# Kernel optimization log

Measured on AMD Instinct MI355X. Metric: run time of the kernel, lower is better.

Reference implementation:

```python
import jax, jax.numpy as jnp
import numpy as np

E4M3_MAX = 448.0
IGNORE = -1000.0
ROTARY_BASE = 10000.0


def quant_dequant_e4m3(w):
    """Emulate per-tensor FP8 E4M3 quantize->dequantize (3 mantissa bits, max 448)."""
    amax = jnp.max(jnp.abs(w))
    scale = E4M3_MAX / jnp.maximum(amax, 1e-12)
    v = w * scale
    a = jnp.abs(v)
    # exponent clipped to E4M3 range (min normal exp -6, max 8)
    e = jnp.clip(jnp.floor(jnp.log2(jnp.maximum(a, 1e-30))), -6.0, 8.0)
    step = jnp.exp2(e - 3.0)  # 3 mantissa bits
    q = jnp.clip(jnp.round(v / step) * step, -E4M3_MAX, E4M3_MAX)
    return (q / scale).astype(w.dtype)


def rotary_sin_cos(rotary_dim, n_ctx):
    pos = jnp.arange(n_ctx, dtype=jnp.float32)
    dim = jnp.arange(rotary_dim // 2, dtype=jnp.float32)
    inv_freq = ROTARY_BASE ** (-dim / (rotary_dim / 2))
    ang = pos[:, None] * inv_freq[None, :]            # [n_ctx, rotary_dim//2]
    ang = jnp.concatenate([ang, ang], axis=-1)        # [n_ctx, rotary_dim]
    return jnp.sin(ang), jnp.cos(ang)


def apply_rotary(x, sin, cos, rotary_dim):
    # x: [B, S, H, Dh]; rotate first rotary_dim dims with rotate-half convention
    S = x.shape[1]
    x_rot, x_pass = x[..., :rotary_dim], x[..., rotary_dim:]
    half = rotary_dim // 2
    x_flip = jnp.concatenate([-x_rot[..., half:], x_rot[..., :half]], axis=-1)
    c = cos[:S][None, :, None, :]
    s = sin[:S][None, :, None, :]
    out = x_rot * c + x_flip * s
    return jnp.concatenate([out, x_pass], axis=-1) if rotary_dim < x.shape[-1] else out


def setup_inputs() -> dict:
    key = jax.random.key(0)
    ks = jax.random.split(key, 8)
    B, S, D, H, Dh = 2, 2048, 1024, 16, 64
    return {
        "query_input": jax.random.normal(ks[0], (B, S, D), jnp.float32),
        "key_input": jax.random.normal(ks[1], (B, S, D), jnp.float32),
        "value_input": jax.random.normal(ks[2], (B, S, D), jnp.float32),
        "W_Q": jax.random.normal(ks[3], (H, D, Dh), jnp.float32) * 0.02,
        "W_K": jax.random.normal(ks[4], (H, D, Dh), jnp.float32) * 0.02,
        "W_V": jax.random.normal(ks[5], (H, D, Dh), jnp.float32) * 0.02,
        "W_O": jax.random.normal(ks[6], (H, Dh, D), jnp.float32) * 0.02,
        "b_Q": jnp.zeros((H, Dh), jnp.float32),
        "b_K": jnp.zeros((H, Dh), jnp.float32),
        "b_V": jnp.zeros((H, Dh), jnp.float32),
        "b_O": jnp.zeros((D,), jnp.float32),
    }


def reference(query_input, key_input, value_input, W_Q, W_K, W_V, W_O, b_Q, b_K, b_V, b_O):
    B, S, D = query_input.shape
    H, _, Dh = W_Q.shape
    rotary_dim = Dh
    attn_scale = jnp.sqrt(jnp.asarray(Dh, jnp.float32))

    # FP8-quantized QKV weights/biases (E4M3 quant-dequant emulation)
    Wq = quant_dequant_e4m3(W_Q)
    Wk = quant_dequant_e4m3(W_K)
    Wv = quant_dequant_e4m3(W_V)
    bq = quant_dequant_e4m3(b_Q)
    bk = quant_dequant_e4m3(b_K)
    bv = quant_dequant_e4m3(b_V)

    q = jnp.einsum("bsd,hde->bshe", query_input, Wq) + bq  # [B,S,H,Dh]
    k = jnp.einsum("bsd,hde->bshe", key_input, Wk) + bk
    v = jnp.einsum("bsd,hde->bshe", value_input, Wv) + bv

    sin, cos = rotary_sin_cos(rotary_dim, S)
    q = apply_rotary(q, sin, cos, rotary_dim)
    k = apply_rotary(k, sin, cos, rotary_dim)

    scores = jnp.einsum("bqhe,bkhe->bhqk", q, k) / attn_scale  # [B,H,S,S]
    causal = jnp.tril(jnp.ones((S, S), bool))
    scores = jnp.where(causal[None, None], scores, IGNORE)
    pattern = jax.nn.softmax(scores, axis=-1)

    z = jnp.einsum("bhqk,bkhe->bqhe", pattern, v)             # [B,S,H,Dh]
    out = jnp.einsum("bqhe,hed->bqd", z, W_O) + b_O           # [B,S,D]
    return out
```

## Files before the change

### kernel.cpp

```cpp
#include <hip/hip_runtime.h>
#include <math.h>


typedef __attribute__((ext_vector_type(8))) short bf16x8;
typedef __attribute__((ext_vector_type(16))) float f32x16;
typedef __attribute__((ext_vector_type(4))) float f32x4;
typedef __attribute__((ext_vector_type(4))) float f4;

#define E4M3_MAX 448.0f

__device__ inline float bf2f(ushort u) { return __uint_as_float(((unsigned)u) << 16); }
__device__ inline ushort f2bf(float f) {
  unsigned u = __float_as_uint(f);
  return (ushort)((u + 0x7FFF + ((u >> 16) & 1)) >> 16);
}
__device__ inline unsigned pack2bf(float a, float b) {
  unsigned ua = __float_as_uint(a), ub = __float_as_uint(b);
  return ((ua + 0x8000u) >> 16) | ((ub + 0x8000u) & 0xFFFF0000u);
}

__device__ __forceinline__ void gll16(const ushort* g, ushort* l) {
  __builtin_amdgcn_global_load_lds(
      (const __attribute__((address_space(1))) unsigned int*)g,
      (__attribute__((address_space(3))) unsigned int*)l, 16, 0, 0);
}

__device__ inline float qdq_qval(float w, float amax) {
  float scale = E4M3_MAX / fmaxf(amax, 1e-12f);
  float v = w * scale;
  float a = fmaxf(fabsf(v), 1e-30f);
  int ex;
  (void)frexpf(a, &ex);
  float e = fminf(fmaxf((float)(ex - 1), -6.0f), 8.0f);
  float step = exp2f(e - 3.0f);
  float q = rintf(v / step) * step;
  return fminf(fmaxf(q, -E4M3_MAX), E4M3_MAX);
}

__device__ __forceinline__ float redpart64(const float* __restrict__ p, int tid) {
  float v = p[tid & 63];
  #pragma unroll
  for (int o = 32; o > 0; o >>= 1) v = fmaxf(v, __shfl_xor(v, o));
  return v;
}

__global__ __launch_bounds__(256) void prep1(const float* __restrict__ W0,
                                             const float* __restrict__ W1,
                                             const float* __restrict__ W2,
                                             const float* __restrict__ b0,
                                             const float* __restrict__ b1,
                                             const float* __restrict__ b2,
                                             const float* __restrict__ Xq,
                                             const float* __restrict__ Xk,
                                             const float* __restrict__ Xv,
                                             float* __restrict__ amaxpart,
                                             ushort* __restrict__ xq,
                                             ushort* __restrict__ xk,
                                             ushort* __restrict__ xv) {
  __shared__ float wred[4];
  int bid = blockIdx.x, tid = threadIdx.x;
  if (bid < 384) {
    int y = bid >> 6, xb = bid & 63;
    const float* src = (y == 0) ? W0 : (y == 1) ? W1 : (y == 2) ? W2
                     : (y == 3) ? b0 : (y == 4) ? b1 : b2;
    int n = (y < 3) ? 1048576 : 1024;
    float m = 0.0f;
    for (int i = xb * 256 + tid; i < n; i += 64 * 256)
      m = fmaxf(m, fabsf(src[i]));
    #pragma unroll
    for (int off = 32; off > 0; off >>= 1)
      m = fmaxf(m, __shfl_xor(m, off));
    if ((tid & 63) == 0) wred[tid >> 6] = m;
    __syncthreads();
    if (tid == 0)
      amaxpart[y * 64 + xb] = fmaxf(fmaxf(wred[0], wred[1]), fmaxf(wred[2], wred[3]));
  } else {
    int t = bid - 384;
    int y = t >> 12, xb = t & 4095;
    const float* in = (y == 0) ? Xq : (y == 1) ? Xk : Xv;
    ushort* out = (y == 0) ? xq : (y == 1) ? xk : xv;
    int i = xb * 256 + tid;
    f4 v = *(const f4*)(in + (size_t)i * 4);
    uint2 o;
    o.x = (unsigned)f2bf(v[0]) | ((unsigned)f2bf(v[1]) << 16);
    o.y = (unsigned)f2bf(v[2]) | ((unsigned)f2bf(v[3]) << 16);
    *(uint2*)(out + (size_t)i * 4) = o;
  }
}

__global__ __launch_bounds__(256) void prep2(const float* __restrict__ W0,
                                             const float* __restrict__ W1,
                                             const float* __restrict__ W2,
                                             const float* __restrict__ WO,
                                             const float* __restrict__ b0,
                                             const float* __restrict__ b1,
                                             const float* __restrict__ b2,
                                             const float* __restrict__ amaxpart,
                                             float* __restrict__ amax,
                                             ushort* __restrict__ o0,
                                             ushort* __restrict__ o1,
                                             ushort* __restrict__ o2,
                                             ushort* __restrict__ woT,
                                             float* __restrict__ bq,
                                             float* __restrict__ bk,
                                             float* __restrict__ bv) {
  __shared__ float tile[64][65];
  int bid = blockIdx.x, tid = threadIdx.x;
  if (bid < 768) {
    int z = bid >> 8, r = bid & 255, hh = r >> 4, xb = r & 15;
    const float* W = (z == 0) ? W0 : (z == 1) ? W1 : W2;
    ushort* Bt = (z == 0) ? o0 : (z == 1) ? o1 : o2;
    float am = redpart64(amaxpart + z * 64, tid);
    if (r == 0 && tid == 0) amax[z] = am;
    int d0 = xb * 64;
    int e = tid & 63, dd = tid >> 6;
    #pragma unroll
    for (int p = 0; p < 16; p++)
      tile[dd + p * 4][e] = W[(size_t)hh * 65536 + (size_t)(d0 + dd + p * 4) * 64 + e];
    __syncthreads();
    int d = tid & 63, ee = tid >> 6;
    #pragma unroll
    for (int p = 0; p < 16; p++) {
      int e2 = ee + p * 4;
      Bt[(size_t)(hh * 64 + e2) * 1024 + d0 + d] = f2bf(qdq_qval(tile[d][e2], am));
    }
  } else if (bid < 780) {
    int q = bid - 768, y = q >> 2, xb = q & 3;
    const float* b = (y == 0) ? b0 : (y == 1) ? b1 : b2;
    float* o = (y == 0) ? bq : (y == 1) ? bk : bv;
    float am = redpart64(amaxpart + (3 + y) * 64, tid);
    int idx = xb * 256 + tid;
    if (idx < 1024) {
      float qv = qdq_qval(b[idx], am);
      o[idx] = qv * (fmaxf(am, 1e-12f) * (1.0f / E4M3_MAX));
    }
  } else {
    int t = bid - 780;
    int xb = t & 15, yb = t >> 4;
    int d0 = xb * 64, he0 = yb * 64;
    int dcol = tid & 63, hr = tid >> 6;
    #pragma unroll
    for (int p = 0; p < 16; p++)
      tile[hr + p * 4][dcol] = WO[(size_t)(he0 + hr + p * 4) * 1024 + d0 + dcol];
    __syncthreads();
    int hcol = tid & 63, dr = tid >> 6;
    #pragma unroll
    for (int p = 0; p < 16; p++)
      woT[(size_t)(d0 + dr + p * 4) * 1024 + he0 + hcol] = f2bf(tile[hcol][dr + p * 4]);
  }
}

template <int QUANT, int TN>
__device__ __forceinline__ void gemm_body(const ushort* __restrict__ A,
                                          const ushort* __restrict__ Bt,
                                          const float* __restrict__ bias, float s_inv,
                                          ushort* __restrict__ outb, float* __restrict__ outf,
                                          int bx, int by, ushort* As, ushort* Bs, int rot) {
  const int K = 1024, N = 1024;
  const int JF = TN / 32;
  int tid = threadIdx.x;
  int w = tid >> 6, lane = tid & 63, quad = lane >> 4, l16 = lane & 15;
  int wm = w & 1, wn = w >> 1;
  int row0 = by * 128, col0 = bx * TN;
  f32x4 acc[4][4] = {};

  for (int k0 = 0; k0 < K; k0 += 64) {
    __syncthreads();
    {
      #pragma unroll
      for (int p = 0; p < 4; p++) {
        int u = tid + p * 256;
        int r = u >> 3, c = u & 7, cs = c ^ (r & 7);
        gll16(&A[(size_t)(row0 + r) * K + k0 + cs * 8], &As[u * 8]);
      }
      #pragma unroll
      for (int p = 0; p < TN / 32; p++) {
        int u = tid + p * 256;
        int r = u >> 3, c = u & 7, cs = c ^ (r & 7);
        gll16(&Bt[(size_t)(col0 + r) * K + k0 + cs * 8], &Bs[u * 8]);
      }
    }
    __syncthreads();
    #pragma unroll
    for (int kk = 0; kk < 2; kk++) {
      bf16x8 af[4], bfr[JF];
      #pragma unroll
      for (int i = 0; i < 4; i++) {
        int arow = wm * 64 + i * 16 + l16;
        af[i] = *(const bf16x8*)&As[arow * 64 + (((kk * 4 + quad) ^ (arow & 7)) * 8)];
      }
      #pragma unroll
      for (int j = 0; j < JF; j++) {
        int brow = wn * (TN / 2) + j * 16 + l16;
        bfr[j] = *(const bf16x8*)&Bs[brow * 64 + (((kk * 4 + quad) ^ (brow & 7)) * 8)];
      }
      #pragma unroll
      for (int i = 0; i < 4; i++)
        #pragma unroll
        for (int j = 0; j < JF; j++)
          acc[i][j] = __builtin_amdgcn_mfma_f32_16x16x32_bf16(af[i], bfr[j], acc[i][j], 0, 0, 0);
    }
  }

  if (QUANT && rot) {
    float bv0[4];
    #pragma unroll
    for (int j = 0; j < 4; j++) bv0[j] = bias[col0 + wn * 64 + j * 16 + l16];
    #pragma unroll
    for (int jp = 0; jp < 2; jp++) {
      float invf = exp2f((float)(jp * 16 + l16) * (-13.287712379549449f / 32.0f));
      int collo = col0 + wn * 64 + jp * 16 + l16;
      #pragma unroll
      for (int i = 0; i < 4; i++) {
        #pragma unroll
        for (int r = 0; r < 4; r++) {
          int row = row0 + wm * 64 + i * 16 + quad * 4 + r;
          float ang = (float)(row & 2047) * invf;
          float sn = __sinf(ang), c = __cosf(ang);
          float lo = acc[i][jp][r] * s_inv + bv0[jp];
          float hi = acc[i][jp + 2][r] * s_inv + bv0[jp + 2];
          outb[(size_t)row * N + collo] = f2bf(lo * c - hi * sn);
          outb[(size_t)row * N + collo + 32] = f2bf(hi * c + lo * sn);
        }
      }
    }
  } else {
    #pragma unroll
    for (int j = 0; j < JF; j++) {
      int col = col0 + wn * (TN / 2) + j * 16 + l16;
      float bv = bias[col];
      #pragma unroll
      for (int i = 0; i < 4; i++) {
        int row = row0 + wm * 64 + i * 16 + quad * 4;
        #pragma unroll
        for (int r = 0; r < 4; r++) {
          float v = acc[i][j][r] * s_inv + bv;
          if (QUANT) outb[(size_t)(row + r) * N + col] = f2bf(v);
          else       outf[(size_t)(row + r) * N + col] = v;
        }
      }
    }
  }
}

__global__ __launch_bounds__(256) void gemm3_qkv(const ushort* __restrict__ xq,
                                                 const ushort* __restrict__ xk,
                                                 const ushort* __restrict__ xv,
                                                 const ushort* __restrict__ wq,
                                                 const ushort* __restrict__ wk,
                                                 const ushort* __restrict__ wv,
                                                 const float* __restrict__ bq,
                                                 const float* __restrict__ bk,
                                                 const float* __restrict__ bv,
                                                 const float* __restrict__ amax,
                                                 ushort* __restrict__ oq,
                                                 ushort* __restrict__ ok,
                                                 ushort* __restrict__ ov) {
  __shared__ ushort As[8192], Bs[8192];
  int z = blockIdx.z;
  const ushort* A  = (z == 0) ? xq : (z == 1) ? xk : xv;
  const ushort* Bt = (z == 0) ? wq : (z == 1) ? wk : wv;
  const float* bias = (z == 0) ? bq : (z == 1) ? bk : bv;
  ushort* out = (z == 0) ? oq : (z == 1) ? ok : ov;
  float s_inv = fmaxf(amax[z], 1e-12f) * (1.0f / E4M3_MAX);
  gemm_body<1, 128>(A, Bt, bias, s_inv, out, nullptr, blockIdx.x, blockIdx.y, As, Bs,
                    (z < 2) ? 1 : 0);
}

__global__ __launch_bounds__(256) void gemm_wo(const ushort* __restrict__ A,
                                               const ushort* __restrict__ Bt,
                                               const float* __restrict__ bias,
                                               float* __restrict__ out) {
  __shared__ ushort As[8192], Bs[4096];
  gemm_body<0, 64>(A, Bt, bias, 1.0f, nullptr, out, blockIdx.x, blockIdx.y, As, Bs, 0);
}

__global__ __launch_bounds__(256) void v_trans(const ushort* __restrict__ v,
                                               ushort* __restrict__ vT) {
  __shared__ ushort tile[64][72];
  int t = blockIdx.x, tid = threadIdx.x;
  int sx = t & 31, h = (t >> 5) & 15, b = t >> 9;
  int s0 = sx * 64;
  int e = tid & 63, sr = tid >> 6;
  #pragma unroll
  for (int p = 0; p < 16; p++)
    tile[sr + p * 4][e] = v[(size_t)(b * 2048 + s0 + sr + p * 4) * 1024 + h * 64 + e];
  __syncthreads();
  int sc = tid & 63, er = tid >> 6;
  #pragma unroll
  for (int p = 0; p < 16; p++)
    vT[(size_t)((b * 16 + h) * 64 + er + p * 4) * 2048 + s0 + sc] = tile[sc][er + p * 4];
}

__global__ __launch_bounds__(512, 4) void flash_mfma9(const ushort* __restrict__ qb,
                                                      const ushort* __restrict__ kb,
                                                      const ushort* __restrict__ vT,
                                                      ushort* __restrict__ zb) {
  int h = blockIdx.y, b = blockIdx.z;
  int tid = threadIdx.x;
  int w8 = tid >> 6;
  int g = w8 >> 2;
  int w = w8 & 3;
  int lane = tid & 63, h2 = lane >> 5, l31 = lane & 31;
  __shared__ ushort sbuf[16384 + 18432];
  ushort* Ks = sbuf + g * 4096;
  ushort* Vs = sbuf + 8192 + g * 4096;
  ushort* P2 = sbuf + 16384 + g * 9216;

  const int qrow = w * 32 + l31;
  const float CE = 0.125f;

  const int ts = tid & 255;
  const int u0 = ts, u1 = ts + 256;
  const int r0 = u0 >> 3, c0 = u0 & 7, r1 = u1 >> 3, c1 = u1 & 7;
  const int sw0 = (c0 ^ (r0 & 7)) * 8, sw1 = (c1 ^ (r1 & 7)) * 8;

  const int qt = (blockIdx.z == 0) ? (int)blockIdx.x : 15 - (int)blockIdx.x;
  const int q0 = qt * 128;
  const int qg = q0 + w * 32 + l31;
  size_t qbase = ((size_t)(b * 2048 + qg)) * 1024 + (size_t)h * 64;
  bf16x8 qf[4];
  #pragma unroll
  for (int ck = 0; ck < 4; ck++)
    qf[ck] = *(const bf16x8*)&qb[qbase + ck * 16 + h2 * 8];

  f32x16 accO[2] = {};
  float mrun = -INFINITY, lrun = 0.0f;

  const int nt = qt + 1;
  const int kt0 = g * nt;

  const ushort* ksrc0 = kb + ((size_t)(b * 2048 + kt0 * 64 + r0)) * 1024 + (size_t)h * 64 + c0 * 8;
  const ushort* ksrc1 = kb + ((size_t)(b * 2048 + kt0 * 64 + r1)) * 1024 + (size_t)h * 64 + c1 * 8;
  const ushort* vsrc0 = vT + ((size_t)((b * 16 + h) * 64 + r0)) * 2048 + kt0 * 64 + c0 * 8;
  const ushort* vsrc1 = vT + ((size_t)((b * 16 + h) * 64 + r1)) * 2048 + kt0 * 64 + c1 * 8;

  uint4 kc0 = *(const uint4*)ksrc0;
  uint4 kc1 = *(const uint4*)ksrc1;
  uint4 vc0 = *(const uint4*)vsrc0;
  uint4 vc1 = *(const uint4*)vsrc1;

  for (int t = 0; t < nt; t++) {
    int kt = kt0 + t;
    __syncthreads();
    *(uint4*)&Ks[r0 * 64 + sw0] = kc0;
    *(uint4*)&Ks[r1 * 64 + sw1] = kc1;
    *(uint4*)&Vs[r0 * 64 + sw0] = vc0;
    *(uint4*)&Vs[r1 * 64 + sw1] = vc1;
    __syncthreads();
    if (t + 1 < nt) {
      kc0 = *(const uint4*)(ksrc0 + (size_t)(t + 1) * 65536);
      kc1 = *(const uint4*)(ksrc1 + (size_t)(t + 1) * 65536);
      vc0 = *(const uint4*)(vsrc0 + (t + 1) * 64);
      vc1 = *(const uint4*)(vsrc1 + (t + 1) * 64);
    }

    bool active = (kt * 64 <= q0 + w * 32 + 31);
    if (active) {
      f32x16 sc[2] = {};
      #pragma unroll
      for (int mf = 0; mf < 2; mf++) {
        int row = mf * 32 + l31;
        int s8 = row & 7;
        #pragma unroll
        for (int ck = 0; ck < 4; ck++) {
          bf16x8 ka = *(const bf16x8*)&Ks[row * 64 + (((2 * ck + h2) ^ s8) * 8)];
          sc[mf] = __builtin_amdgcn_mfma_f32_32x32x16_bf16(ka, qf[ck], sc[mf], 0, 0, 0);
        }
      }

      if (kt * 64 + 63 > q0 + w * 32) {
        #pragma unroll
        for (int mf = 0; mf < 2; mf++)
          #pragma unroll
          for (int i = 0; i < 16; i++) {
            int kv = kt * 64 + mf * 32 + (i & 3) + 8 * (i >> 2) + 4 * h2;
            sc[mf][i] = (kv > qg) ? -8000.0f : sc[mf][i];
          }
      }

      float tm = sc[0][0];
      #pragma unroll
      for (int i = 1; i < 16; i++) tm = fmaxf(tm, sc[0][i]);
      #pragma unroll
      for (int i = 0; i < 16; i++) tm = fmaxf(tm, sc[1][i]);
      tm = fmaxf(tm, __shfl_xor(tm, 32));
      float mnew = fmaxf(mrun, tm);
      float alpha = __expf((mrun - mnew) * CE);
      float p[2][16];
      float rs = 0.0f;
      #pragma unroll
      for (int mf = 0; mf < 2; mf++)
        #pragma unroll
        for (int i = 0; i < 16; i++) {
          float pv = __expf((sc[mf][i] - mnew) * CE);
          p[mf][i] = pv;
          rs += pv;
        }
      rs += __shfl_xor(rs, 32);
      lrun = lrun * alpha + rs;
      mrun = mnew;
      #pragma unroll
      for (int mf = 0; mf < 2; mf++)
        #pragma unroll
        for (int i = 0; i < 16; i++) accO[mf][i] *= alpha;

      #pragma unroll
      for (int mf = 0; mf < 2; mf++)
        #pragma unroll
        for (int m = 0; m < 4; m++) {
          uint2 w2;
          w2.x = pack2bf(p[mf][4 * m + 0], p[mf][4 * m + 1]);
          w2.y = pack2bf(p[mf][4 * m + 2], p[mf][4 * m + 3]);
          *(uint2*)&P2[qrow * 72 + 32 * mf + 8 * m + 4 * h2] = w2;
        }

      #pragma unroll
      for (int ck = 0; ck < 4; ck++) {
        bf16x8 pB = *(const bf16x8*)&P2[qrow * 72 + ck * 16 + h2 * 8];
        #pragma unroll
        for (int mf = 0; mf < 2; mf++) {
          int row = mf * 32 + l31;
          bf16x8 va = *(const bf16x8*)&Vs[row * 64 + (((2 * ck + h2) ^ (row & 7)) * 8)];
          accO[mf] = __builtin_amdgcn_mfma_f32_32x32x16_bf16(va, pB, accO[mf], 0, 0, 0);
        }
      }
    }
  }

  __syncthreads();
  float* mbuf = (float*)sbuf;
  int midx = (w * 64 + lane) * 35;
  if (g == 1) {
    #pragma unroll
    for (int i = 0; i < 16; i++) mbuf[midx + i] = accO[0][i];
    #pragma unroll
    for (int i = 0; i < 16; i++) mbuf[midx + 16 + i] = accO[1][i];
    mbuf[midx + 32] = mrun;
    mbuf[midx + 33] = lrun;
  }
  __syncthreads();
  ushort* Osb = sbuf + 16384 + 9216;
  if (g == 0) {
    float m1 = mbuf[midx + 32], l1 = mbuf[midx + 33];
    float mn = fmaxf(mrun, m1);
    float a0 = __expf((mrun - mn) * CE), a1 = __expf((m1 - mn) * CE);
    float linv = 1.0f / (lrun * a0 + l1 * a1);
    #pragma unroll
    for (int mf = 0; mf < 2; mf++)
      #pragma unroll
      for (int m = 0; m < 4; m++) {
        int e0 = 32 * mf + 8 * m + 4 * h2;
        float o0 = (accO[mf][4 * m + 0] * a0 + mbuf[midx + 16 * mf + 4 * m + 0] * a1) * linv;
        float o1 = (accO[mf][4 * m + 1] * a0 + mbuf[midx + 16 * mf + 4 * m + 1] * a1) * linv;
        float o2 = (accO[mf][4 * m + 2] * a0 + mbuf[midx + 16 * mf + 4 * m + 2] * a1) * linv;
        float o3 = (accO[mf][4 * m + 3] * a0 + mbuf[midx + 16 * mf + 4 * m + 3] * a1) * linv;
        *(unsigned*)&Osb[qrow * 72 + e0] = pack2bf(o0, o1);
        *(unsigned*)&Osb[qrow * 72 + e0 + 2] = pack2bf(o2, o3);
      }
  }
  __syncthreads();
  size_t obase = ((size_t)(b * 2048 + q0)) * 1024 + (size_t)h * 64;
  #pragma unroll
  for (int i = 0; i < 2; i++) {
    int u = tid + i * 512;
    int r = u >> 3, blk = u & 7;
    *(uint4*)&zb[obase + (size_t)r * 1024 + blk * 8] = *(const uint4*)&Osb[r * 72 + blk * 8];
  }
}

extern "C" void kernel_launch(void* const* d_in, const int* in_sizes, int n_in,
                              void* d_out, int out_size, void* d_ws, size_t ws_size,
                              hipStream_t stream) {
  const float* Xq  = (const float*)d_in[0];
  const float* Xk  = (const float*)d_in[1];
  const float* Xv  = (const float*)d_in[2];
  const float* W_Q = (const float*)d_in[3];
  const float* W_K = (const float*)d_in[4];
  const float* W_V = (const float*)d_in[5];
  const float* W_O = (const float*)d_in[6];
  const float* b_Q = (const float*)d_in[7];
  const float* b_K = (const float*)d_in[8];
  const float* b_V = (const float*)d_in[9];
  const float* b_O = (const float*)d_in[10];
  float* out = (float*)d_out;

  char* base = (char*)d_ws;
  float*  amax = (float*)(base + 0);
  float*  amaxpart = (float*)(base + 1024);
  float*  bq   = (float*)(base + 4096);
  float*  bk   = (float*)(base + 8192);
  float*  bv   = (float*)(base + 12288);
  ushort* wq   = (ushort*)(base + 16384);
  ushort* wk   = (ushort*)(base + 16384 + 2097152);
  ushort* wv   = (ushort*)(base + 16384 + 2u * 2097152);
  ushort* woT  = (ushort*)(base + 16384 + 3u * 2097152);
  ushort* xq   = (ushort*)(base + 8404992);
  ushort* xk   = (ushort*)(base + 16793600);
  ushort* xv   = (ushort*)(base + 25182208);
  ushort* qbf  = (ushort*)(base + 33570816);
  ushort* kbf  = (ushort*)(base + 41959424);
  ushort* vbf  = (ushort*)(base + 50348032);
  ushort* vT   = xq;
  ushort* zbf  = xk;

  prep1<<<12672, 256, 0, stream>>>(W_Q, W_K, W_V, b_Q, b_K, b_V, Xq, Xk, Xv,
                                   amaxpart, xq, xk, xv);
  prep2<<<1036, 256, 0, stream>>>(W_Q, W_K, W_V, W_O, b_Q, b_K, b_V,
                                  amaxpart, amax, wq, wk, wv, woT, bq, bk, bv);
  dim3 g3(8, 32, 3);
  gemm3_qkv<<<g3, 256, 0, stream>>>(xq, xk, xv, wq, wk, wv, bq, bk, bv, amax,
                                    qbf, kbf, vbf);
  v_trans<<<1024, 256, 0, stream>>>(vbf, vT);
  dim3 fgrid(16, 16, 2);
  flash_mfma9<<<fgrid, 512, 0, stream>>>(qbf, kbf, vT, zbf);
  dim3 wog(16, 32);
  gemm_wo<<<wog, 256, 0, stream>>>(zbf, woT, b_O, out);
}
```

Before: 238.6 us.

## Fuse V transpose into QKV GEMM epilogue and remap GEMM block order

The V projection epilogue now stages its bf16 tile in LDS and writes it out transposed as [b,h,e,s] with 16-byte stores, so the separate v_trans kernel and its extra global round trip are gone. The QKV and WO GEMMs also switch to 1D grids with a swizzled block-to-tile mapping, which groups blocks that share operand tiles to improve L2 reuse. The cost is an extra LDS pass and two barriers in the V epilogue, plus a larger shared buffer that may reduce occupancy.

```diff
diff --git a/kernel.cpp b/kernel.cpp
--- a/kernel.cpp
+++ b/kernel.cpp
@@ -150,12 +150,12 @@
   }
 }
 
-template <int QUANT, int TN>
+template <int MODE, int TN>
 __device__ __forceinline__ void gemm_body(const ushort* __restrict__ A,
                                           const ushort* __restrict__ Bt,
                                           const float* __restrict__ bias, float s_inv,
                                           ushort* __restrict__ outb, float* __restrict__ outf,
-                                          int bx, int by, ushort* As, ushort* Bs, int rot) {
+                                          int bx, int by, ushort* As, ushort* Bs) {
   const int K = 1024, N = 1024;
   const int JF = TN / 32;
   int tid = threadIdx.x;
@@ -202,7 +202,7 @@
     }
   }
 
-  if (QUANT && rot) {
+  if (MODE == 2) {
     float bv0[4];
     #pragma unroll
     for (int j = 0; j < 4; j++) bv0[j] = bias[col0 + wn * 64 + j * 16 + l16];
@@ -224,6 +224,33 @@
         }
       }
     }
+  } else if (MODE == 3) {
+    __syncthreads();
+    ushort* sb = As;
+    #pragma unroll
+    for (int j = 0; j < JF; j++) {
+      int colL = wn * (TN / 2) + j * 16 + l16;
+      float bv = bias[col0 + colL];
+      #pragma unroll
+      for (int i = 0; i < 4; i++) {
+        int rowL = wm * 64 + i * 16 + quad * 4;
+        uint2 o;
+        o.x = (unsigned)f2bf(acc[i][j][0] * s_inv + bv) |
+              ((unsigned)f2bf(acc[i][j][1] * s_inv + bv) << 16);
+        o.y = (unsigned)f2bf(acc[i][j][2] * s_inv + bv) |
+              ((unsigned)f2bf(acc[i][j][3] * s_inv + bv) << 16);
+        *(uint2*)&sb[colL * 136 + rowL] = o;
+      }
+    }
+    __syncthreads();
+    int bb = row0 >> 11, sloc = row0 & 2047;
+    #pragma unroll
+    for (int p = 0; p < 8; p++) {
+      int u = tid + p * 256;
+      int r = u >> 4, cc = u & 15;
+      *(uint4*)&outb[(size_t)(bb * 1024 + col0 + r) * 2048 + sloc + cc * 8] =
+          *(const uint4*)&sb[r * 136 + cc * 8];
+    }
   } else {
     #pragma unroll
     for (int j = 0; j < JF; j++) {
@@ -233,11 +260,8 @@
       for (int i = 0; i < 4; i++) {
         int row = row0 + wm * 64 + i * 16 + quad * 4;
         #pragma unroll
-        for (int r = 0; r < 4; r++) {
-          float v = acc[i][j][r] * s_inv + bv;
-          if (QUANT) outb[(size_t)(row + r) * N + col] = f2bf(v);
-          else       outf[(size_t)(row + r) * N + col] = v;
-        }
+        for (int r = 0; r < 4; r++)
+          outf[(size_t)(row + r) * N + col] = acc[i][j][r] * s_inv + bv;
       }
     }
   }
@@ -255,41 +279,33 @@
                                                  const float* __restrict__ amax,
                                                  ushort* __restrict__ oq,
                                                  ushort* __restrict__ ok,
-                                                 ushort* __restrict__ ov) {
-  __shared__ ushort As[8192], Bs[8192];
-  int z = blockIdx.z;
+                                                 ushort* __restrict__ vT) {
+  __shared__ __align__(16) ushort sb[17408];
+  ushort* As = sb;
+  ushort* Bs = sb + 8192;
+  int bid = blockIdx.x;
+  int rr = bid & 7, t = bid >> 3;
+  int bx = t & 7, gq = rr + 8 * (t >> 3);
+  int by = gq & 31, z = gq >> 5;
   const ushort* A  = (z == 0) ? xq : (z == 1) ? xk : xv;
   const ushort* Bt = (z == 0) ? wq : (z == 1) ? wk : wv;
   const float* bias = (z == 0) ? bq : (z == 1) ? bk : bv;
-  ushort* out = (z == 0) ? oq : (z == 1) ? ok : ov;
   float s_inv = fmaxf(amax[z], 1e-12f) * (1.0f / E4M3_MAX);
-  gemm_body<1, 128>(A, Bt, bias, s_inv, out, nullptr, blockIdx.x, blockIdx.y, As, Bs,
-                    (z < 2) ? 1 : 0);
+  if (z == 2)
+    gemm_body<3, 128>(A, Bt, bias, s_inv, vT, nullptr, bx, by, As, Bs);
+  else
+    gemm_body<2, 128>(A, Bt, bias, s_inv, (z == 0) ? oq : ok, nullptr, bx, by, As, Bs);
 }
 
 __global__ __launch_bounds__(256) void gemm_wo(const ushort* __restrict__ A,
                                                const ushort* __restrict__ Bt,
                                                const float* __restrict__ bias,
                                                float* __restrict__ out) {
-  __shared__ ushort As[8192], Bs[4096];
-  gemm_body<0, 64>(A, Bt, bias, 1.0f, nullptr, out, blockIdx.x, blockIdx.y, As, Bs, 0);
-}
-
-__global__ __launch_bounds__(256) void v_trans(const ushort* __restrict__ v,
-                                               ushort* __restrict__ vT) {
-  __shared__ ushort tile[64][72];
-  int t = blockIdx.x, tid = threadIdx.x;
-  int sx = t & 31, h = (t >> 5) & 15, b = t >> 9;
-  int s0 = sx * 64;
-  int e = tid & 63, sr = tid >> 6;
-  #pragma unroll
-  for (int p = 0; p < 16; p++)
-    tile[sr + p * 4][e] = v[(size_t)(b * 2048 + s0 + sr + p * 4) * 1024 + h * 64 + e];
-  __syncthreads();
-  int sc = tid & 63, er = tid >> 6;
-  #pragma unroll
-  for (int p = 0; p < 16; p++)
-    vT[(size_t)((b * 16 + h) * 64 + er + p * 4) * 2048 + s0 + sc] = tile[sc][er + p * 4];
+  __shared__ __align__(16) ushort As[8192], Bs[4096];
+  int bid = blockIdx.x;
+  int rr = bid & 7, t = bid >> 3;
+  int bx = t & 15, by = rr + 8 * (t >> 4);
+  gemm_body<0, 64>(A, Bt, bias, 1.0f, nullptr, out, bx, by, As, Bs);
 }
 
 __global__ __launch_bounds__(512, 4) void flash_mfma9(const ushort* __restrict__ qb,
@@ -500,20 +516,16 @@
   ushort* xv   = (ushort*)(base + 25182208);
   ushort* qbf  = (ushort*)(base + 33570816);
   ushort* kbf  = (ushort*)(base + 41959424);
-  ushort* vbf  = (ushort*)(base + 50348032);
-  ushort* vT   = xq;
+  ushort* vT   = (ushort*)(base + 50348032);
   ushort* zbf  = xk;
 
   prep1<<<12672, 256, 0, stream>>>(W_Q, W_K, W_V, b_Q, b_K, b_V, Xq, Xk, Xv,
                                    amaxpart, xq, xk, xv);
   prep2<<<1036, 256, 0, stream>>>(W_Q, W_K, W_V, W_O, b_Q, b_K, b_V,
                                   amaxpart, amax, wq, wk, wv, woT, bq, bk, bv);
-  dim3 g3(8, 32, 3);
-  gemm3_qkv<<<g3, 256, 0, stream>>>(xq, xk, xv, wq, wk, wv, bq, bk, bv, amax,
-                                    qbf, kbf, vbf);
-  v_trans<<<1024, 256, 0, stream>>>(vbf, vT);
+  gemm3_qkv<<<768, 256, 0, stream>>>(xq, xk, xv, wq, wk, wv, bq, bk, bv, amax,
+                                     qbf, kbf, vT);
   dim3 fgrid(16, 16, 2);
   flash_mfma9<<<fgrid, 512, 0, stream>>>(qbf, kbf, vT, zbf);
-  dim3 wog(16, 32);
-  gemm_wo<<<wog, 256, 0, stream>>>(zbf, woT, b_O, out);
-}
+  gemm_wo<<<512, 256, 0, stream>>>(zbf, woT, b_O, out);
+}
```

Result: faster. 229.0 us (-4.0%).
